# Optimization experiments

Measured on AMD Instinct MI355X. Metric: run time of the kernel, lower is better.

## Reference

```python
import jax, jax.numpy as jnp
import numpy as np

B, D, H = 64, 768, 512            # batch, bert hidden, classifier hidden_dim
G0, C0 = 8192, 8                  # level-0 meta labels, children per meta
G1, C1 = 65536, 11                # level-1 meta labels, children per meta (incl. pad)
L = 670091                        # num labels; pad id == L, table has L+1 rows
K1, K2 = 32, 64                   # candidates_topk


def setup_inputs() -> dict:
    key = jax.random.key(0)
    ks = jax.random.split(key, 14)
    rn = lambda k, shp, s=1.0: jax.random.normal(k, shp, jnp.float32) * s
    w = 0.02  # xavier-ish init scale
    inp = {
        'feat5':   rn(ks[0], (B, D)),
        'feat8':   rn(ks[1], (B, D)),
        'featcat': rn(ks[2], (B, 3 * D)),
        'W0': rn(ks[3], (D, H), w),     'b0': jnp.zeros((H,), jnp.float32),
        'W1': rn(ks[4], (D, H), w),     'b1': jnp.zeros((H,), jnp.float32),
        'W2': rn(ks[5], (3 * D, H), w), 'b2': jnp.zeros((H,), jnp.float32),
        'E0': rn(ks[6], (G0, H), w),
        'E1': rn(ks[7], (G1, H), w),
        # padding row (index L) is zero, per self.Cn[-1].weight[-1].data.fill_(0)
        'E2': rn(ks[8], (L + 1, H), w).at[-1].set(0.0),
        'g0': jax.random.randint(ks[9], (G0, C0), 0, G1, dtype=jnp.int32),
        'g1': jax.random.randint(ks[10], (G1, C1), 0, L + 1, dtype=jnp.int32),
    }
    return inp


def reference(feat5, feat8, featcat, W0, b0, W1, b1, W2, b2, E0, E1, E2, g0, g1):
    gelu = lambda x: jax.nn.gelu(x, approximate=False)  # torch nn.GELU default (erf)
    # Cn_hidden (dropout is identity at eval)
    h0 = gelu(feat5 @ W0 + b0)      # [B,H]
    h1 = gelu(feat8 @ W1 + b1)      # [B,H]
    h2 = gelu(featcat @ W2 + b2)    # [B,H]

    # ---- level 0: score all G0 meta-labels (dense bmm) ----
    logits0 = jnp.einsum('gh,bh->bg', E0, h0)            # [B,G0]
    p0 = jax.nn.sigmoid(logits0)
    prev0 = jax.lax.stop_gradient(p0)                    # prev_logits = scores.detach()

    # ---- level 1: topk routing + gather + bmm ----
    sc1, idx1 = jax.lax.top_k(prev0, K1)                 # [B,K1]; prev_cands is arange -> identity map
    cands1 = g0[idx1].reshape(B, K1 * C0)                # [B,K1*C0] level-1 meta ids
    gsc1 = jnp.repeat(sc1, C0, axis=1)                   # candidates_scores flattened
    logits1 = jnp.einsum('bch,bh->bc', E1[cands1], h1)   # [B,K1*C0]
    p1 = jax.nn.sigmoid(logits1)
    w1 = p1 * gsc1
    prev1 = jax.lax.stop_gradient(p1)

    # ---- level 2 (final): topk routing into padded label groups ----
    sc2, idx2 = jax.lax.top_k(prev1, K2)                 # [B,K2]
    meta2 = jnp.take_along_axis(cands1, idx2, axis=1)    # indices into g1
    cands2 = g1[meta2].reshape(B, K2 * C1)               # [B,K2*C1] label ids (L == pad)
    gsc2 = jnp.repeat(sc2, C1, axis=1)
    logits2 = jnp.einsum('bch,bh->bc', E2[cands2], h2)   # pad rows of E2 are 0 -> logit 0
    # torch: where(logits==0, -inf, logits).sigmoid() -> pad positions score 0
    p2 = jnp.where(logits2 == 0.0, jnp.float32(0.0), jax.nn.sigmoid(logits2))
    w2 = p2 * gsc2

    return (p0, p1, p2, w1, w2, cands1, cands2)
```

## Files before the change

kernel.cpp:

```cpp
#include <hip/hip_runtime.h>
#include <math.h>

#define BB 64
#define D0 768
#define D2 2304
#define HH 512
#define BBHH (BB*HH)
#define NG0 8192
#define NC0 8
#define NCH1 11
#define TK1 32
#define TK2 64
#define NC1 (TK1*NC0)
#define NC2 (TK2*NCH1)
#define SPA 2
#define SPB 2
#define SPC 18
#define NSL (SPA+SPB+SPC)

__device__ __forceinline__ float sigmoidf_(float x){ return 1.0f/(1.0f+expf(-x)); }
__device__ __forceinline__ float geluf_(float x){ return 0.5f*x*(1.0f+erff(x*0.70710678118654752f)); }
__device__ __forceinline__ unsigned long long maxu64_(unsigned long long a, unsigned long long b){ return a>b?a:b; }

__device__ __forceinline__ unsigned long long bitonic256_desc(
    unsigned long long key, int tid, unsigned long long* sbuf)
{
  #pragma unroll
  for (int k = 2; k <= 256; k <<= 1) {
    #pragma unroll
    for (int j = k >> 1; j > 0; j >>= 1) {
      unsigned long long other;
      if (j >= 64) {
        __syncthreads();
        sbuf[tid] = key;
        __syncthreads();
        other = sbuf[tid ^ j];
      } else {
        other = __shfl_xor(key, j, 64);
      }
      bool keep_max = ((tid & j) == 0) == ((tid & k) == 0);
      key = keep_max ? (key > other ? key : other)
                     : (key < other ? key : other);
    }
  }
  return key;
}

__global__ __launch_bounds__(256) void gemm_h_kernel(
    const float* __restrict__ feat5, const float* __restrict__ feat8,
    const float* __restrict__ featcat,
    const float* __restrict__ W0, const float* __restrict__ W1,
    const float* __restrict__ W2, float* __restrict__ P)
{
  __shared__ __align__(16) float At[32][68];
  __shared__ __align__(16) float Bt[32][68];
  const int bid = blockIdx.x, tid = threadIdx.x;
  if (bid < 64) {
    const float* X = (bid < 32) ? feat5 : feat8;
    const float* W = (bid < 32) ? W0 : W1;
    int l = bid & 31;
    int split = l & 1, jt = (l >> 1) * 32;
    float* Pb = P + (size_t)((bid < 32 ? 0 : SPA) + split)*BBHH;
    int k0 = split*384;
    int ti = tid >> 4, tj = tid & 15;
    float acc[4][2] = {};
    for (int ks = 0; ks < 384; ks += 32) {
      #pragma unroll
      for (int it = 0; it < 2; ++it) {
        int q = tid + it*256;
        int b = q & 63, kq = q >> 6;
        float4 v = *(const float4*)(X + (size_t)b*D0 + k0 + ks + kq*4);
        At[kq*4+0][b]=v.x; At[kq*4+1][b]=v.y; At[kq*4+2][b]=v.z; At[kq*4+3][b]=v.w;
      }
      {
        int j4 = tid & 7, kk = tid >> 3;
        float4 v = *(const float4*)(W + (size_t)(k0+ks+kk)*HH + jt + j4*4);
        *(float4*)&Bt[kk][j4*4] = v;
      }
      __syncthreads();
      #pragma unroll
      for (int k = 0; k < 32; ++k) {
        float4 a = *(const float4*)&At[k][ti*4];
        float2 b = *(const float2*)&Bt[k][tj*2];
        float av[4] = {a.x,a.y,a.z,a.w};
        float bv[2] = {b.x,b.y};
        #pragma unroll
        for (int r=0;r<4;++r)
          #pragma unroll
          for (int c=0;c<2;++c) acc[r][c] += av[r]*bv[c];
      }
      __syncthreads();
    }
    #pragma unroll
    for (int r=0;r<4;++r)
      #pragma unroll
      for (int c=0;c<2;++c)
        Pb[(size_t)(ti*4+r)*HH + jt + tj*2 + c] = acc[r][c];
  } else {
    int l = bid - 64;
    int split = l % 18, tile = l / 18;
    float* Pb = P + (size_t)(SPA+SPB+split)*BBHH;
    int k0 = split*128;
    int jt = tile*64;
    int ti = tid >> 4, tj = tid & 15;
    float acc[4][4] = {};
    for (int ks = 0; ks < 128; ks += 32) {
      #pragma unroll
      for (int it = 0; it < 2; ++it) {
        int q = tid + it*256;
        int b = q & 63, kq = q >> 6;
        float4 v = *(const float4*)(featcat + (size_t)b*D2 + k0 + ks + kq*4);
        At[kq*4+0][b]=v.x; At[kq*4+1][b]=v.y; At[kq*4+2][b]=v.z; At[kq*4+3][b]=v.w;
      }
      #pragma unroll
      for (int it = 0; it < 2; ++it) {
        int q = tid + it*256;
        int j4 = q & 15, kk = q >> 4;
        float4 v = *(const float4*)(W2 + (size_t)(k0+ks+kk)*HH + jt + j4*4);
        *(float4*)&Bt[kk][j4*4] = v;
      }
      __syncthreads();
      #pragma unroll
      for (int k = 0; k < 32; ++k) {
        float4 a = *(const float4*)&At[k][ti*4];
        float4 b = *(const float4*)&Bt[k][tj*4];
        float av[4] = {a.x,a.y,a.z,a.w};
        float bv[4] = {b.x,b.y,b.z,b.w};
        #pragma unroll
        for (int r=0;r<4;++r)
          #pragma unroll
          for (int c=0;c<4;++c) acc[r][c] += av[r]*bv[c];
      }
      __syncthreads();
    }
    #pragma unroll
    for (int r=0;r<4;++r)
      #pragma unroll
      for (int c=0;c<4;++c)
        Pb[(size_t)(ti*4+r)*HH + jt + tj*4 + c] = acc[r][c];
  }
}

__global__ __launch_bounds__(256) void level0_kernel(
    const float* __restrict__ P, const float* __restrict__ b0v,
    const float* __restrict__ E0, float* __restrict__ p0out)
{
  __shared__ __align__(16) float At[32][36];
  __shared__ __align__(16) float Bt[32][68];
  const int bid = blockIdx.x, tid = threadIdx.x;
  int btile = bid & 1;
  int gt = bid >> 1;
  int ti = tid >> 4, tj = tid & 15;
  float acc[2][4] = {};
  for (int ks = 0; ks < HH; ks += 32) {
    {
      int bb = tid & 31, kq = tid >> 5;
      float4 a = make_float4(0.f,0.f,0.f,0.f);
      #pragma unroll
      for (int s=0;s<SPA;++s){
        const float4 p = *(const float4*)(P + (size_t)s*BBHH
                           + (size_t)(btile*32+bb)*HH + ks + kq*4);
        a.x+=p.x; a.y+=p.y; a.z+=p.z; a.w+=p.w;
      }
      float4 bv = *(const float4*)(b0v + ks + kq*4);
      At[kq*4+0][bb]=geluf_(a.x+bv.x);
      At[kq*4+1][bb]=geluf_(a.y+bv.y);
      At[kq*4+2][bb]=geluf_(a.z+bv.z);
      At[kq*4+3][bb]=geluf_(a.w+bv.w);
    }
    #pragma unroll
    for (int it=0; it<2; ++it) {
      int q = tid + it*256; int g = q & 63, kq = q >> 6;
      float4 v = *(const float4*)(E0 + (size_t)(gt*64+g)*HH + ks + kq*4);
      Bt[kq*4+0][g]=v.x; Bt[kq*4+1][g]=v.y; Bt[kq*4+2][g]=v.z; Bt[kq*4+3][g]=v.w;
    }
    __syncthreads();
    #pragma unroll
    for (int k=0;k<32;++k) {
      float2 a = *(const float2*)&At[k][ti*2];
      float4 b = *(const float4*)&Bt[k][tj*4];
      float av[2] = {a.x,a.y};
      float bv[4] = {b.x,b.y,b.z,b.w};
      #pragma unroll
      for (int r=0;r<2;++r)
        #pragma unroll
        for (int c=0;c<4;++c) acc[r][c] += av[r]*bv[c];
    }
    __syncthreads();
  }
  #pragma unroll
  for (int r=0;r<2;++r)
    #pragma unroll
    for (int c=0;c<4;++c)
      p0out[(size_t)(btile*32 + ti*2 + r)*NG0 + gt*64 + tj*4 + c] = sigmoidf_(acc[r][c]);
}

__global__ __launch_bounds__(256) void topk1_level1_kernel(
    const float* __restrict__ p0, const int* __restrict__ g0,
    const float* __restrict__ P, const float* __restrict__ b1v,
    const float* __restrict__ E1,
    int* __restrict__ cands1_i, float* __restrict__ o_c1,
    float* __restrict__ o_p1, float* __restrict__ o_w1)
{
  const int bid = blockIdx.x, tid = threadIdx.x;
  const int b = bid & 63, q = bid >> 6;
  const int lane = tid & 63, wid = tid >> 6;
  __shared__ float h1row[HH];
  __shared__ unsigned long long sbuf[256];
  __shared__ unsigned long long slist[256];
  __shared__ float s_sc[TK1];
  __shared__ int   s_idx[TK1];
  __shared__ int   scnt;
  {
    int j = tid*2;
    float ax=0.f, ay=0.f;
    #pragma unroll
    for (int s=0;s<SPB;++s){
      float2 v = *(const float2*)(P + (size_t)(SPA+s)*BBHH + (size_t)b*HH + j);
      ax += v.x; ay += v.y;
    }
    float2 bv = *(const float2*)(b1v + j);
    h1row[j]   = geluf_(ax + bv.x);
    h1row[j+1] = geluf_(ay + bv.y);
  }
  if (tid==0) scnt = 0;
  const float* row = p0 + (size_t)b*NG0;
  const float4* rp = (const float4*)(row + tid*32);
  unsigned long long m = 0ull;
  #pragma unroll
  for (int t=0;t<8;++t){
    float4 v = rp[t];
    unsigned i0 = (unsigned)(tid*32 + t*4);
    m = maxu64_(m, ((unsigned long long)__float_as_uint(v.x)<<32) | (unsigned long long)(0xFFFFFFFFu-(i0+0)));
    m = maxu64_(m, ((unsigned long long)__float_as_uint(v.y)<<32) | (unsigned long long)(0xFFFFFFFFu-(i0+1)));
    m = maxu64_(m, ((unsigned long long)__float_as_uint(v.z)<<32) | (unsigned long long)(0xFFFFFFFFu-(i0+2)));
    m = maxu64_(m, ((unsigned long long)__float_as_uint(v.w)<<32) | (unsigned long long)(0xFFFFFFFFu-(i0+3)));
  }
  __syncthreads();
  unsigned long long sk = bitonic256_desc(m, tid, sbuf);
  __syncthreads();
  sbuf[tid] = sk;
  __syncthreads();
  unsigned long long t32 = sbuf[31];
  __syncthreads();
  #pragma unroll
  for (int t=0;t<8;++t){
    float4 v = rp[t];
    unsigned i0 = (unsigned)(tid*32 + t*4);
    unsigned long long k0 = ((unsigned long long)__float_as_uint(v.x)<<32) | (unsigned long long)(0xFFFFFFFFu-(i0+0));
    unsigned long long k1 = ((unsigned long long)__float_as_uint(v.y)<<32) | (unsigned long long)(0xFFFFFFFFu-(i0+1));
    unsigned long long k2 = ((unsigned long long)__float_as_uint(v.z)<<32) | (unsigned long long)(0xFFFFFFFFu-(i0+2));
    unsigned long long k3 = ((unsigned long long)__float_as_uint(v.w)<<32) | (unsigned long long)(0xFFFFFFFFu-(i0+3));
    if (k0 >= t32) { int p = atomicAdd(&scnt,1); if (p<256) slist[p]=k0; }
    if (k1 >= t32) { int p = atomicAdd(&scnt,1); if (p<256) slist[p]=k1; }
    if (k2 >= t32) { int p = atomicAdd(&scnt,1); if (p<256) slist[p]=k2; }
    if (k3 >= t32) { int p = atomicAdd(&scnt,1); if (p<256) slist[p]=k3; }
  }
  __syncthreads();
  int cnt = scnt;
  unsigned long long key2 = (tid < cnt) ? slist[tid] : 0ull;
  key2 = bitonic256_desc(key2, tid, sbuf);
  __syncthreads();
  sbuf[tid] = key2;
  __syncthreads();
  if (tid < TK1) {
    unsigned long long w = sbuf[tid];
    s_idx[tid] = (int)(0xFFFFFFFFu - (unsigned)(w & 0xFFFFFFFFull));
    s_sc[tid]  = __uint_as_float((unsigned)(w>>32));
  }
  __syncthreads();
  if (q==0 && tid < NC1) {
    int k = tid >> 3, c = tid & 7;
    int cand = g0[(size_t)s_idx[k]*NC0 + c];
    cands1_i[(size_t)b*NC1+tid] = cand;
    o_c1[(size_t)b*NC1+tid] = (float)cand;
  }
  float4 ha = *(const float4*)&h1row[lane*8];
  float4 hb = *(const float4*)&h1row[lane*8+4];
  #pragma unroll
  for (int j=0;j<4;++j){
    int cbase = (q + 4*j)*16 + wid*4;
    int id0 = g0[(size_t)s_idx[(cbase+0)>>3]*NC0 + ((cbase+0)&7)];
    int id1 = g0[(size_t)s_idx[(cbase+1)>>3]*NC0 + ((cbase+1)&7)];
    int id2 = g0[(size_t)s_idx[(cbase+2)>>3]*NC0 + ((cbase+2)&7)];
    int id3 = g0[(size_t)s_idx[(cbase+3)>>3]*NC0 + ((cbase+3)&7)];
    const float4* pe0 = (const float4*)(E1 + (size_t)id0*HH);
    const float4* pe1 = (const float4*)(E1 + (size_t)id1*HH);
    const float4* pe2 = (const float4*)(E1 + (size_t)id2*HH);
    const float4* pe3 = (const float4*)(E1 + (size_t)id3*HH);
    float4 a0=pe0[lane*2], c0=pe0[lane*2+1];
    float4 a1=pe1[lane*2], c1=pe1[lane*2+1];
    float4 a2=pe2[lane*2], c2=pe2[lane*2+1];
    float4 a3=pe3[lane*2], c3=pe3[lane*2+1];
    float s0 = ha.x*a0.x+ha.y*a0.y+ha.z*a0.z+ha.w*a0.w + hb.x*c0.x+hb.y*c0.y+hb.z*c0.z+hb.w*c0.w;
    float s1 = ha.x*a1.x+ha.y*a1.y+ha.z*a1.z+ha.w*a1.w + hb.x*c1.x+hb.y*c1.y+hb.z*c1.z+hb.w*c1.w;
    float s2 = ha.x*a2.x+ha.y*a2.y+ha.z*a2.z+ha.w*a2.w + hb.x*c2.x+hb.y*c2.y+hb.z*c2.z+hb.w*c2.w;
    float s3 = ha.x*a3.x+ha.y*a3.y+ha.z*a3.z+ha.w*a3.w + hb.x*c3.x+hb.y*c3.y+hb.z*c3.z+hb.w*c3.w;
    #pragma unroll
    for (int off=1; off<64; off<<=1) {
      s0 += __shfl_xor(s0, off);
      s1 += __shfl_xor(s1, off);
      s2 += __shfl_xor(s2, off);
      s3 += __shfl_xor(s3, off);
    }
    if (lane==0) {
      float p;
      p = sigmoidf_(s0); o_p1[(size_t)b*NC1+cbase+0]=p; o_w1[(size_t)b*NC1+cbase+0]=p*s_sc[(cbase+0)>>3];
      p = sigmoidf_(s1); o_p1[(size_t)b*NC1+cbase+1]=p; o_w1[(size_t)b*NC1+cbase+1]=p*s_sc[(cbase+1)>>3];
      p = sigmoidf_(s2); o_p1[(size_t)b*NC1+cbase+2]=p; o_w1[(size_t)b*NC1+cbase+2]=p*s_sc[(cbase+2)>>3];
      p = sigmoidf_(s3); o_p1[(size_t)b*NC1+cbase+3]=p; o_w1[(size_t)b*NC1+cbase+3]=p*s_sc[(cbase+3)>>3];
    }
  }
}

__global__ __launch_bounds__(256) void topk2_level2_kernel(
    const float* __restrict__ p1, const int* __restrict__ cands1_i,
    const int* __restrict__ g1,
    const float* __restrict__ P, const float* __restrict__ b2v,
    const float* __restrict__ E2,
    float* __restrict__ o_c2, float* __restrict__ o_p2, float* __restrict__ o_w2)
{
  const int bid = blockIdx.x, tid = threadIdx.x;
  const int b = bid & 63, q = bid >> 6;
  const int lane = tid & 63, wid = tid >> 6;
  __shared__ float h2row[HH];
  __shared__ unsigned long long sbuf[256];
  __shared__ float s_sc[TK2];
  __shared__ int   s_idx[TK2];
  __shared__ int   c1row[NC1];
  {
    int j = tid*2;
    float ax=0.f, ay=0.f;
    #pragma unroll
    for (int s=0;s<SPC;++s){
      float2 v = *(const float2*)(P + (size_t)(SPA+SPB+s)*BBHH + (size_t)b*HH + j);
      ax += v.x; ay += v.y;
    }
    float2 bv = *(const float2*)(b2v + j);
    h2row[j]   = geluf_(ax + bv.x);
    h2row[j+1] = geluf_(ay + bv.y);
  }
  c1row[tid] = cands1_i[(size_t)b*NC1 + tid];
  float v = p1[(size_t)b*NC1 + tid];
  unsigned long long key = ((unsigned long long)__float_as_uint(v)<<32) |
                           (unsigned long long)(0xFFFFFFFFu - (unsigned)tid);
  __syncthreads();
  key = bitonic256_desc(key, tid, sbuf);
  __syncthreads();
  sbuf[tid] = key;
  __syncthreads();
  if (tid < TK2) {
    unsigned long long w = sbuf[tid];
    s_idx[tid] = (int)(0xFFFFFFFFu - (unsigned)(w & 0xFFFFFFFFull));
    s_sc[tid]  = __uint_as_float((unsigned)(w>>32));
  }
  __syncthreads();
  if (q==0) {
    for (int e=tid; e<NC2; e+=256) {
      int k = e/NCH1, c = e - k*NCH1;
      int meta = c1row[s_idx[k]];
      int cand = g1[(size_t)meta*NCH1 + c];
      o_c2[(size_t)b*NC2+e] = (float)cand;
    }
  }
  float4 ha = *(const float4*)&h2row[lane*8];
  float4 hb = *(const float4*)&h2row[lane*8+4];
  #pragma unroll
  for (int j=0;j<11;++j){
    int cbase = (q + 4*j)*16 + wid*4;
    int k0i = (cbase+0)/NCH1, c0i = (cbase+0) - k0i*NCH1;
    int k1i = (cbase+1)/NCH1, c1i = (cbase+1) - k1i*NCH1;
    int k2i = (cbase+2)/NCH1, c2i = (cbase+2) - k2i*NCH1;
    int k3i = (cbase+3)/NCH1, c3i = (cbase+3) - k3i*NCH1;
    int id0 = g1[(size_t)c1row[s_idx[k0i]]*NCH1 + c0i];
    int id1 = g1[(size_t)c1row[s_idx[k1i]]*NCH1 + c1i];
    int id2 = g1[(size_t)c1row[s_idx[k2i]]*NCH1 + c2i];
    int id3 = g1[(size_t)c1row[s_idx[k3i]]*NCH1 + c3i];
    const float4* pe0 = (const float4*)(E2 + (size_t)id0*HH);
    const float4* pe1 = (const float4*)(E2 + (size_t)id1*HH);
    const float4* pe2 = (const float4*)(E2 + (size_t)id2*HH);
    const float4* pe3 = (const float4*)(E2 + (size_t)id3*HH);
    float4 a0=pe0[lane*2], c0=pe0[lane*2+1];
    float4 a1=pe1[lane*2], c1=pe1[lane*2+1];
    float4 a2=pe2[lane*2], c2=pe2[lane*2+1];
    float4 a3=pe3[lane*2], c3=pe3[lane*2+1];
    float s0 = ha.x*a0.x+ha.y*a0.y+ha.z*a0.z+ha.w*a0.w + hb.x*c0.x+hb.y*c0.y+hb.z*c0.z+hb.w*c0.w;
    float s1 = ha.x*a1.x+ha.y*a1.y+ha.z*a1.z+ha.w*a1.w + hb.x*c1.x+hb.y*c1.y+hb.z*c1.z+hb.w*c1.w;
    float s2 = ha.x*a2.x+ha.y*a2.y+ha.z*a2.z+ha.w*a2.w + hb.x*c2.x+hb.y*c2.y+hb.z*c2.z+hb.w*c2.w;
    float s3 = ha.x*a3.x+ha.y*a3.y+ha.z*a3.z+ha.w*a3.w + hb.x*c3.x+hb.y*c3.y+hb.z*c3.z+hb.w*c3.w;
    #pragma unroll
    for (int off=1; off<64; off<<=1) {
      s0 += __shfl_xor(s0, off);
      s1 += __shfl_xor(s1, off);
      s2 += __shfl_xor(s2, off);
      s3 += __shfl_xor(s3, off);
    }
    if (lane==0) {
      float p;
      p = (s0==0.0f)?0.0f:sigmoidf_(s0); o_p2[(size_t)b*NC2+cbase+0]=p; o_w2[(size_t)b*NC2+cbase+0]=p*s_sc[k0i];
      p = (s1==0.0f)?0.0f:sigmoidf_(s1); o_p2[(size_t)b*NC2+cbase+1]=p; o_w2[(size_t)b*NC2+cbase+1]=p*s_sc[k1i];
      p = (s2==0.0f)?0.0f:sigmoidf_(s2); o_p2[(size_t)b*NC2+cbase+2]=p; o_w2[(size_t)b*NC2+cbase+2]=p*s_sc[k2i];
      p = (s3==0.0f)?0.0f:sigmoidf_(s3); o_p2[(size_t)b*NC2+cbase+3]=p; o_w2[(size_t)b*NC2+cbase+3]=p*s_sc[k3i];
    }
  }
}

extern "C" void kernel_launch(void* const* d_in, const int* in_sizes, int n_in,
                              void* d_out, int out_size, void* d_ws, size_t ws_size,
                              hipStream_t stream) {
  const float* feat5   = (const float*)d_in[0];
  const float* feat8   = (const float*)d_in[1];
  const float* featcat = (const float*)d_in[2];
  const float* W0 = (const float*)d_in[3];
  const float* b0 = (const float*)d_in[4];
  const float* W1 = (const float*)d_in[5];
  const float* b1 = (const float*)d_in[6];
  const float* W2 = (const float*)d_in[7];
  const float* b2 = (const float*)d_in[8];
  const float* E0 = (const float*)d_in[9];
  const float* E1 = (const float*)d_in[10];
  const float* E2 = (const float*)d_in[11];
  const int*   g0 = (const int*)d_in[12];
  const int*   g1 = (const int*)d_in[13];

  float* out = (float*)d_out;
  float* ws  = (float*)d_ws;

  size_t off = 0;
  float* P = ws + off; off += (size_t)NSL*BBHH;
  int*   cands1_i = (int*)(ws + off); off += (size_t)BB*NC1;

  float* o_p0 = out;
  float* o_p1 = o_p0 + (size_t)BB*NG0;
  float* o_p2 = o_p1 + (size_t)BB*NC1;
  float* o_w1 = o_p2 + (size_t)BB*NC2;
  float* o_w2 = o_w1 + (size_t)BB*NC1;
  float* o_c1 = o_w2 + (size_t)BB*NC2;
  float* o_c2 = o_c1 + (size_t)BB*NC1;

  gemm_h_kernel<<<dim3(208), dim3(256), 0, stream>>>(feat5, feat8, featcat, W0, W1, W2, P);
  level0_kernel<<<dim3(256), dim3(256), 0, stream>>>(P, b0, E0, o_p0);
  topk1_level1_kernel<<<dim3(256), dim3(256), 0, stream>>>(o_p0, g0, P, b1, E1,
      cands1_i, o_c1, o_p1, o_w1);
  topk2_level2_kernel<<<dim3(256), dim3(256), 0, stream>>>(o_p1, cands1_i, g1, P, b2, E2,
      o_c2, o_p2, o_w2);
}
```

Before: 100.8 us.

## Rebalance work splits across the hidden GEMM, level-0 scoring and level-2 scoring kernels

The hidden-layer GEMM now uses one code path for all three inputs. The featcat projection uses 6 K-splits of 384 with 32-column tiles instead of 18 splits of 128, so downstream kernels sum fewer partial slices. The level-0 kernel uses 16-row batch tiles over 512 blocks with a 1x4 register tile per thread. The level-2 kernel launches 512 blocks, each scoring 2 candidates per wave per iteration. All three aim to raise occupancy and parallelism and to cut partial-sum traffic. The risk is that every extra level-2 block per row repeats the per-row top-k selection, and the smaller GEMM tiles reuse less data.

```diff
diff --git a/kernel.cpp b/kernel.cpp
--- a/kernel.cpp
+++ b/kernel.cpp
@@ -15,7 +15,7 @@
 #define NC2 (TK2*NCH1)
 #define SPA 2
 #define SPB 2
-#define SPC 18
+#define SPC 6
 #define NSL (SPA+SPB+SPC)
 
 __device__ __forceinline__ float sigmoidf_(float x){ return 1.0f/(1.0f+expf(-x)); }
@@ -53,120 +53,74 @@
     const float* __restrict__ W2, float* __restrict__ P)
 {
   __shared__ __align__(16) float At[32][68];
+  __shared__ __align__(16) float Bt[32][36];
+  const int bid = blockIdx.x, tid = threadIdx.x;
+  const float* X; const float* W; int Dm, split, jt, slice;
+  if (bid < 32)      { X=feat5;   W=W0; Dm=D0; int l=bid;    split=l&1; jt=(l>>1)*32; slice=split; }
+  else if (bid < 64) { X=feat8;   W=W1; Dm=D0; int l=bid-32; split=l&1; jt=(l>>1)*32; slice=SPA+split; }
+  else               { X=featcat; W=W2; Dm=D2; int l=bid-64; split=l%6; jt=(l/6)*32;  slice=SPA+SPB+split; }
+  float* Pb = P + (size_t)slice*BBHH;
+  int k0 = split*384;
+  int ti = tid >> 4, tj = tid & 15;
+  float acc[4][2] = {};
+  for (int ks = 0; ks < 384; ks += 32) {
+    #pragma unroll
+    for (int it = 0; it < 2; ++it) {
+      int q = tid + it*256;
+      int b = q & 63, kq = q >> 6;
+      float4 v = *(const float4*)(X + (size_t)b*Dm + k0 + ks + kq*4);
+      At[kq*4+0][b]=v.x; At[kq*4+1][b]=v.y; At[kq*4+2][b]=v.z; At[kq*4+3][b]=v.w;
+    }
+    {
+      int j4 = tid & 7, kk = tid >> 3;
+      float4 v = *(const float4*)(W + (size_t)(k0+ks+kk)*HH + jt + j4*4);
+      *(float4*)&Bt[kk][j4*4] = v;
+    }
+    __syncthreads();
+    #pragma unroll
+    for (int k = 0; k < 32; ++k) {
+      float4 a = *(const float4*)&At[k][ti*4];
+      float2 b = *(const float2*)&Bt[k][tj*2];
+      float av[4] = {a.x,a.y,a.z,a.w};
+      float bv[2] = {b.x,b.y};
+      #pragma unroll
+      for (int r=0;r<4;++r)
+        #pragma unroll
+        for (int c=0;c<2;++c) acc[r][c] += av[r]*bv[c];
+    }
+    __syncthreads();
+  }
+  #pragma unroll
+  for (int r=0;r<4;++r)
+    #pragma unroll
+    for (int c=0;c<2;++c)
+      Pb[(size_t)(ti*4+r)*HH + jt + tj*2 + c] = acc[r][c];
+}
+
+__global__ __launch_bounds__(256,2) void level0_kernel(
+    const float* __restrict__ P, const float* __restrict__ b0v,
+    const float* __restrict__ E0, float* __restrict__ p0out)
+{
+  __shared__ __align__(16) float At[32][20];
   __shared__ __align__(16) float Bt[32][68];
   const int bid = blockIdx.x, tid = threadIdx.x;
-  if (bid < 64) {
-    const float* X = (bid < 32) ? feat5 : feat8;
-    const float* W = (bid < 32) ? W0 : W1;
-    int l = bid & 31;
-    int split = l & 1, jt = (l >> 1) * 32;
-    float* Pb = P + (size_t)((bid < 32 ? 0 : SPA) + split)*BBHH;
-    int k0 = split*384;
-    int ti = tid >> 4, tj = tid & 15;
-    float acc[4][2] = {};
-    for (int ks = 0; ks < 384; ks += 32) {
-      #pragma unroll
-      for (int it = 0; it < 2; ++it) {
-        int q = tid + it*256;
-        int b = q & 63, kq = q >> 6;
-        float4 v = *(const float4*)(X + (size_t)b*D0 + k0 + ks + kq*4);
-        At[kq*4+0][b]=v.x; At[kq*4+1][b]=v.y; At[kq*4+2][b]=v.z; At[kq*4+3][b]=v.w;
-      }
-      {
-        int j4 = tid & 7, kk = tid >> 3;
-        float4 v = *(const float4*)(W + (size_t)(k0+ks+kk)*HH + jt + j4*4);
-        *(float4*)&Bt[kk][j4*4] = v;
-      }
-      __syncthreads();
-      #pragma unroll
-      for (int k = 0; k < 32; ++k) {
-        float4 a = *(const float4*)&At[k][ti*4];
-        float2 b = *(const float2*)&Bt[k][tj*2];
-        float av[4] = {a.x,a.y,a.z,a.w};
-        float bv[2] = {b.x,b.y};
-        #pragma unroll
-        for (int r=0;r<4;++r)
-          #pragma unroll
-          for (int c=0;c<2;++c) acc[r][c] += av[r]*bv[c];
-      }
-      __syncthreads();
-    }
-    #pragma unroll
-    for (int r=0;r<4;++r)
-      #pragma unroll
-      for (int c=0;c<2;++c)
-        Pb[(size_t)(ti*4+r)*HH + jt + tj*2 + c] = acc[r][c];
-  } else {
-    int l = bid - 64;
-    int split = l % 18, tile = l / 18;
-    float* Pb = P + (size_t)(SPA+SPB+split)*BBHH;
-    int k0 = split*128;
-    int jt = tile*64;
-    int ti = tid >> 4, tj = tid & 15;
-    float acc[4][4] = {};
-    for (int ks = 0; ks < 128; ks += 32) {
-      #pragma unroll
-      for (int it = 0; it < 2; ++it) {
-        int q = tid + it*256;
-        int b = q & 63, kq = q >> 6;
-        float4 v = *(const float4*)(featcat + (size_t)b*D2 + k0 + ks + kq*4);
-        At[kq*4+0][b]=v.x; At[kq*4+1][b]=v.y; At[kq*4+2][b]=v.z; At[kq*4+3][b]=v.w;
-      }
-      #pragma unroll
-      for (int it = 0; it < 2; ++it) {
-        int q = tid + it*256;
-        int j4 = q & 15, kk = q >> 4;
-        float4 v = *(const float4*)(W2 + (size_t)(k0+ks+kk)*HH + jt + j4*4);
-        *(float4*)&Bt[kk][j4*4] = v;
-      }
-      __syncthreads();
-      #pragma unroll
-      for (int k = 0; k < 32; ++k) {
-        float4 a = *(const float4*)&At[k][ti*4];
-        float4 b = *(const float4*)&Bt[k][tj*4];
-        float av[4] = {a.x,a.y,a.z,a.w};
-        float bv[4] = {b.x,b.y,b.z,b.w};
-        #pragma unroll
-        for (int r=0;r<4;++r)
-          #pragma unroll
-          for (int c=0;c<4;++c) acc[r][c] += av[r]*bv[c];
-      }
-      __syncthreads();
-    }
-    #pragma unroll
-    for (int r=0;r<4;++r)
-      #pragma unroll
-      for (int c=0;c<4;++c)
-        Pb[(size_t)(ti*4+r)*HH + jt + tj*4 + c] = acc[r][c];
-  }
-}
-
-__global__ __launch_bounds__(256) void level0_kernel(
-    const float* __restrict__ P, const float* __restrict__ b0v,
-    const float* __restrict__ E0, float* __restrict__ p0out)
-{
-  __shared__ __align__(16) float At[32][36];
-  __shared__ __align__(16) float Bt[32][68];
-  const int bid = blockIdx.x, tid = threadIdx.x;
-  int btile = bid & 1;
-  int gt = bid >> 1;
-  int ti = tid >> 4, tj = tid & 15;
-  float acc[2][4] = {};
+  const int btile = bid & 3;
+  const int gt = bid >> 2;
+  const int ti = tid >> 4, tj = tid & 15;
+  float acc[4] = {};
   for (int ks = 0; ks < HH; ks += 32) {
     {
-      int bb = tid & 31, kq = tid >> 5;
-      float4 a = make_float4(0.f,0.f,0.f,0.f);
+      int bb = tid & 15, kq = tid >> 4;
+      float2 a = make_float2(0.f, 0.f);
       #pragma unroll
       for (int s=0;s<SPA;++s){
-        const float4 p = *(const float4*)(P + (size_t)s*BBHH
-                           + (size_t)(btile*32+bb)*HH + ks + kq*4);
-        a.x+=p.x; a.y+=p.y; a.z+=p.z; a.w+=p.w;
+        float2 p = *(const float2*)(P + (size_t)s*BBHH
+                        + (size_t)(btile*16+bb)*HH + ks + kq*2);
+        a.x += p.x; a.y += p.y;
       }
-      float4 bv = *(const float4*)(b0v + ks + kq*4);
-      At[kq*4+0][bb]=geluf_(a.x+bv.x);
-      At[kq*4+1][bb]=geluf_(a.y+bv.y);
-      At[kq*4+2][bb]=geluf_(a.z+bv.z);
-      At[kq*4+3][bb]=geluf_(a.w+bv.w);
+      float2 bv = *(const float2*)(b0v + ks + kq*2);
+      At[kq*2+0][bb] = geluf_(a.x + bv.x);
+      At[kq*2+1][bb] = geluf_(a.y + bv.y);
     }
     #pragma unroll
     for (int it=0; it<2; ++it) {
@@ -177,22 +131,15 @@
     __syncthreads();
     #pragma unroll
     for (int k=0;k<32;++k) {
-      float2 a = *(const float2*)&At[k][ti*2];
+      float a = At[k][ti];
       float4 b = *(const float4*)&Bt[k][tj*4];
-      float av[2] = {a.x,a.y};
-      float bv[4] = {b.x,b.y,b.z,b.w};
-      #pragma unroll
-      for (int r=0;r<2;++r)
-        #pragma unroll
-        for (int c=0;c<4;++c) acc[r][c] += av[r]*bv[c];
+      acc[0] += a*b.x; acc[1] += a*b.y; acc[2] += a*b.z; acc[3] += a*b.w;
     }
     __syncthreads();
   }
   #pragma unroll
-  for (int r=0;r<2;++r)
-    #pragma unroll
-    for (int c=0;c<4;++c)
-      p0out[(size_t)(btile*32 + ti*2 + r)*NG0 + gt*64 + tj*4 + c] = sigmoidf_(acc[r][c]);
+  for (int c=0;c<4;++c)
+    p0out[(size_t)(btile*16 + ti)*NG0 + gt*64 + tj*4 + c] = sigmoidf_(acc[c]);
 }
 
 __global__ __launch_bounds__(256) void topk1_level1_kernel(
@@ -313,7 +260,7 @@
   }
 }
 
-__global__ __launch_bounds__(256) void topk2_level2_kernel(
+__global__ __launch_bounds__(256,2) void topk2_level2_kernel(
     const float* __restrict__ p1, const int* __restrict__ cands1_i,
     const int* __restrict__ g1,
     const float* __restrict__ P, const float* __restrict__ b2v,
@@ -365,42 +312,27 @@
   }
   float4 ha = *(const float4*)&h2row[lane*8];
   float4 hb = *(const float4*)&h2row[lane*8+4];
-  #pragma unroll
   for (int j=0;j<11;++j){
-    int cbase = (q + 4*j)*16 + wid*4;
+    int cbase = q*88 + j*8 + wid*2;
     int k0i = (cbase+0)/NCH1, c0i = (cbase+0) - k0i*NCH1;
     int k1i = (cbase+1)/NCH1, c1i = (cbase+1) - k1i*NCH1;
-    int k2i = (cbase+2)/NCH1, c2i = (cbase+2) - k2i*NCH1;
-    int k3i = (cbase+3)/NCH1, c3i = (cbase+3) - k3i*NCH1;
     int id0 = g1[(size_t)c1row[s_idx[k0i]]*NCH1 + c0i];
     int id1 = g1[(size_t)c1row[s_idx[k1i]]*NCH1 + c1i];
-    int id2 = g1[(size_t)c1row[s_idx[k2i]]*NCH1 + c2i];
-    int id3 = g1[(size_t)c1row[s_idx[k3i]]*NCH1 + c3i];
     const float4* pe0 = (const float4*)(E2 + (size_t)id0*HH);
     const float4* pe1 = (const float4*)(E2 + (size_t)id1*HH);
-    const float4* pe2 = (const float4*)(E2 + (size_t)id2*HH);
-    const float4* pe3 = (const float4*)(E2 + (size_t)id3*HH);
     float4 a0=pe0[lane*2], c0=pe0[lane*2+1];
     float4 a1=pe1[lane*2], c1=pe1[lane*2+1];
-    float4 a2=pe2[lane*2], c2=pe2[lane*2+1];
-    float4 a3=pe3[lane*2], c3=pe3[lane*2+1];
     float s0 = ha.x*a0.x+ha.y*a0.y+ha.z*a0.z+ha.w*a0.w + hb.x*c0.x+hb.y*c0.y+hb.z*c0.z+hb.w*c0.w;
     float s1 = ha.x*a1.x+ha.y*a1.y+ha.z*a1.z+ha.w*a1.w + hb.x*c1.x+hb.y*c1.y+hb.z*c1.z+hb.w*c1.w;
-    float s2 = ha.x*a2.x+ha.y*a2.y+ha.z*a2.z+ha.w*a2.w + hb.x*c2.x+hb.y*c2.y+hb.z*c2.z+hb.w*c2.w;
-    float s3 = ha.x*a3.x+ha.y*a3.y+ha.z*a3.z+ha.w*a3.w + hb.x*c3.x+hb.y*c3.y+hb.z*c3.z+hb.w*c3.w;
     #pragma unroll
     for (int off=1; off<64; off<<=1) {
       s0 += __shfl_xor(s0, off);
       s1 += __shfl_xor(s1, off);
-      s2 += __shfl_xor(s2, off);
-      s3 += __shfl_xor(s3, off);
     }
     if (lane==0) {
       float p;
       p = (s0==0.0f)?0.0f:sigmoidf_(s0); o_p2[(size_t)b*NC2+cbase+0]=p; o_w2[(size_t)b*NC2+cbase+0]=p*s_sc[k0i];
       p = (s1==0.0f)?0.0f:sigmoidf_(s1); o_p2[(size_t)b*NC2+cbase+1]=p; o_w2[(size_t)b*NC2+cbase+1]=p*s_sc[k1i];
-      p = (s2==0.0f)?0.0f:sigmoidf_(s2); o_p2[(size_t)b*NC2+cbase+2]=p; o_w2[(size_t)b*NC2+cbase+2]=p*s_sc[k2i];
-      p = (s3==0.0f)?0.0f:sigmoidf_(s3); o_p2[(size_t)b*NC2+cbase+3]=p; o_w2[(size_t)b*NC2+cbase+3]=p*s_sc[k3i];
     }
   }
 }
@@ -438,10 +370,10 @@
   float* o_c1 = o_w2 + (size_t)BB*NC2;
   float* o_c2 = o_c1 + (size_t)BB*NC1;
 
-  gemm_h_kernel<<<dim3(208), dim3(256), 0, stream>>>(feat5, feat8, featcat, W0, W1, W2, P);
-  level0_kernel<<<dim3(256), dim3(256), 0, stream>>>(P, b0, E0, o_p0);
+  gemm_h_kernel<<<dim3(160), dim3(256), 0, stream>>>(feat5, feat8, featcat, W0, W1, W2, P);
+  level0_kernel<<<dim3(512), dim3(256), 0, stream>>>(P, b0, E0, o_p0);
   topk1_level1_kernel<<<dim3(256), dim3(256), 0, stream>>>(o_p0, g0, P, b1, E1,
       cands1_i, o_c1, o_p1, o_w1);
-  topk2_level2_kernel<<<dim3(256), dim3(256), 0, stream>>>(o_p1, cands1_i, g1, P, b2, E2,
+  topk2_level2_kernel<<<dim3(512), dim3(256), 0, stream>>>(o_p1, cands1_i, g1, P, b2, E2,
       o_c2, o_p2, o_w2);
 }
```

Result: faster. 90.05 us (-10.7%).
